# Performance work log

Hardware: AMD Instinct MI355X
Metric: run time of the kernel (lower is better)

## Reference

```python
import jax, jax.numpy as jnp
import numpy as np

B, S, K, H = 512, 128, 4, 128  # batch, seq_len, interest_num, hidden_size
ROUTING_TIMES = 3
EPS = 1e-9


def setup_inputs() -> dict:
    key = jax.random.key(0)
    k1, k2 = jax.random.split(key)
    item_eb = jax.random.normal(k1, (B, S, H), dtype=jnp.float32)
    mask = jnp.ones((B, S), dtype=jnp.float32)
    # learned bilinear map parameter (bilinear_type == 2)
    w = jax.random.normal(k2, (1, S, K * H, H), dtype=jnp.float32) * 0.02
    return {"item_eb": item_eb, "mask": mask, "w": w}


def _squash(cap):
    # cap: [B, K, 1, H]
    n = jnp.sum(cap * cap, axis=-1, keepdims=True)
    return (n / (1.0 + n) / jnp.sqrt(n + EPS)) * cap


def reference(item_eb, mask, w):
    # bilinear_type==2: sum(w[:, :S] * item_eb[:, :, None, :], axis=3)
    # expressed as an einsum to avoid the [B,S,K*H,H] intermediate
    item_eb_hat = jnp.einsum('bsh,sdh->bsd', item_eb, w[0])          # [B, S, K*H]
    item_eb_hat = item_eb_hat.reshape(B, S, K, H).transpose(0, 2, 1, 3)  # [B, K, S, H]
    hat_iter = jax.lax.stop_gradient(item_eb_hat)  # stop_grad=True

    atten_mask = jnp.broadcast_to(mask[:, None, :], (B, K, S))
    capsule_weight = jnp.zeros((B, K, S), dtype=item_eb.dtype)  # bilinear_type > 0

    interest_capsule = None
    for i in range(ROUTING_TIMES):
        # torch F.softmax with implicit dim on a 3D tensor -> dim=0 (legacy)
        sw = jax.nn.softmax(capsule_weight, axis=0)
        sw = jnp.where(atten_mask == 0, 0.0, sw)[:, :, None, :]  # [B, K, 1, S]
        src = hat_iter if i < 2 else item_eb_hat
        interest_capsule = _squash(jnp.matmul(sw, src))  # [B, K, 1, H]
        if i < 2:
            delta = jnp.matmul(hat_iter, interest_capsule.transpose(0, 1, 3, 2))  # [B,K,S,1]
            capsule_weight = capsule_weight + delta.reshape(B, K, S)

    return interest_capsule.reshape(B, K, H)
```

## Files before the change

kernel.cpp:

```cpp
#include <hip/hip_runtime.h>
#include <math.h>

#define BB 512
#define SS 128
#define KK 4
#define HH 128
#define DD 512

typedef __attribute__((ext_vector_type(8))) short bf16x8;
typedef __attribute__((ext_vector_type(4))) float f32x4;

__device__ __forceinline__ unsigned short f2bf(float f) {
  unsigned u = __float_as_uint(f);
  unsigned r = u + 0x7fffu + ((u >> 16) & 1u);
  return (unsigned short)(r >> 16);
}
__device__ __forceinline__ float bfhi(unsigned u) { return __uint_as_float(u & 0xffff0000u); }
__device__ __forceinline__ float bflo(unsigned u) { return __uint_as_float(u << 16); }
__device__ __forceinline__ unsigned pk2(float a, float b) {
  return (unsigned)f2bf(a) | ((unsigned)f2bf(b) << 16);
}

__global__ __launch_bounds__(256) void einsum_mfma(
    const float* __restrict__ A,
    const float* __restrict__ W,
    unsigned short* __restrict__ hat)
{
  __shared__ unsigned short Al[128 * 64];
  __shared__ unsigned short Wl[128 * 64];
  const int s  = blockIdx.x;
  const int b0 = (blockIdx.y & 3) * 128;
  const int dt = blockIdx.y >> 2;
  const int d0 = dt * 128;
  const int t  = threadIdx.x;
  const int lane = t & 63, wv = t >> 6;
  const int qm = wv & 1, qn = wv >> 1;
  const int n16 = lane & 15, kq = lane >> 4;
  const int r = t >> 1, cq = t & 1;

  f32x4 acc[4][4] = {};
  for (int ks = 0; ks < 128; ks += 64) {
    const float* ga = A + ((size_t)(b0 + r) * SS + s) * HH + ks + cq * 32;
    const float* gw = W + ((size_t)s * DD + d0 + r) * HH + ks + cq * 32;
    #pragma unroll
    for (int j = 0; j < 4; j++) {
      float4 a0 = *(const float4*)(ga + 8 * j);
      float4 a1 = *(const float4*)(ga + 8 * j + 4);
      float4 w0 = *(const float4*)(gw + 8 * j);
      float4 w1 = *(const float4*)(gw + 8 * j + 4);
      const int goff = ((cq * 4 + j + r) & 7) * 8;
      uint4 pa, pw;
      pa.x = pk2(a0.x, a0.y); pa.y = pk2(a0.z, a0.w);
      pa.z = pk2(a1.x, a1.y); pa.w = pk2(a1.z, a1.w);
      pw.x = pk2(w0.x, w0.y); pw.y = pk2(w0.z, w0.w);
      pw.z = pk2(w1.x, w1.y); pw.w = pk2(w1.z, w1.w);
      *(uint4*)&Al[r * 64 + goff] = pa;
      *(uint4*)&Wl[r * 64 + goff] = pw;
    }
    __syncthreads();
    #pragma unroll
    for (int kk = 0; kk < 2; kk++) {
      bf16x8 af[4], bfr[4];
      #pragma unroll
      for (int i = 0; i < 4; i++) {
        const int ra = qm * 64 + i * 16 + n16;
        const int rb = qn * 64 + i * 16 + n16;
        af[i]  = *(const bf16x8*)&Wl[ra * 64 + ((kk * 4 + kq + ra) & 7) * 8];
        bfr[i] = *(const bf16x8*)&Al[rb * 64 + ((kk * 4 + kq + rb) & 7) * 8];
      }
      #pragma unroll
      for (int i = 0; i < 4; i++)
        #pragma unroll
        for (int j = 0; j < 4; j++)
          acc[i][j] = __builtin_amdgcn_mfma_f32_16x16x32_bf16(af[i], bfr[j], acc[i][j], 0, 0, 0);
    }
    __syncthreads();
  }

  #pragma unroll
  for (int j = 0; j < 4; j++) {
    const int b = b0 + qn * 64 + j * 16 + n16;
    unsigned short* orow = hat + (((size_t)b * KK + dt) * SS + s) * HH;
    #pragma unroll
    for (int i = 0; i < 4; i++) {
      const int h = qm * 64 + i * 16 + kq * 4;
      ushort4 o;
      o.x = f2bf(acc[i][j][0]); o.y = f2bf(acc[i][j][1]);
      o.z = f2bf(acc[i][j][2]); o.w = f2bf(acc[i][j][3]);
      *(ushort4*)(orow + h) = o;
    }
  }
}

__global__ __launch_bounds__(256) void softmax_k(
    const float* __restrict__ cw, float* __restrict__ sw)
{
  __shared__ float T[512 * 33];
  __shared__ float red[2][8][32];
  const int s0 = blockIdx.x * 32, k = blockIdx.y, t = threadIdx.x;
  const int bg = t >> 3, c = t & 7;

  #pragma unroll
  for (int i = 0; i < 16; i++) {
    const int b = i * 32 + bg;
    float4 v = *(const float4*)(cw + ((size_t)b * KK + k) * SS + s0 + c * 4);
    float* Tr = &T[b * 33 + c * 4];
    Tr[0] = v.x; Tr[1] = v.y; Tr[2] = v.z; Tr[3] = v.w;
  }
  __syncthreads();

  const int sc = t & 31, grp = t >> 5;
  float mx = -3.4e38f;
  #pragma unroll 8
  for (int i = 0; i < 64; i++)
    mx = fmaxf(mx, T[(grp * 64 + i) * 33 + sc]);
  red[0][grp][sc] = mx;
  __syncthreads();
  float mall = red[0][0][sc];
  #pragma unroll
  for (int g = 1; g < 8; g++) mall = fmaxf(mall, red[0][g][sc]);
  float sm = 0.f;
  #pragma unroll 8
  for (int i = 0; i < 64; i++) {
    float* p = &T[(grp * 64 + i) * 33 + sc];
    float e = __expf(*p - mall);
    *p = e; sm += e;
  }
  red[1][grp][sc] = sm;
  __syncthreads();
  float tot = 0.f;
  #pragma unroll
  for (int g = 0; g < 8; g++) tot += red[1][g][sc];
  const float inv = 1.f / tot;
  #pragma unroll 8
  for (int i = 0; i < 64; i++)
    T[(grp * 64 + i) * 33 + sc] *= inv;
  __syncthreads();

  #pragma unroll
  for (int i = 0; i < 16; i++) {
    const int b = i * 32 + bg;
    const float* Tr = &T[b * 33 + c * 4];
    *(float4*)(sw + ((size_t)b * KK + k) * SS + s0 + c * 4) =
        make_float4(Tr[0], Tr[1], Tr[2], Tr[3]);
  }
}

__global__ __launch_bounds__(256) void routing_k(
    const unsigned short* __restrict__ hat, const float* __restrict__ mask,
    const float* __restrict__ sw_in, float* __restrict__ cw,
    float* __restrict__ out, int mode)
{
  __shared__ unsigned short hat_l[128 * 136];
  __shared__ float sw_l[128];
  __shared__ float4 red4[8][32];
  __shared__ float4 cq4[32];
  const int b = blockIdx.x, k = blockIdx.y, t = threadIdx.x;

  if (t < 128) {
    const float mk = mask[(size_t)b * SS + t];
    sw_l[t] = (mode == 0)
      ? ((mk == 0.f) ? 0.f : (1.f / 512.f))
      : ((mk == 0.f) ? 0.f : sw_in[((size_t)b * KK + k) * SS + t]);
  }
  const uint4* hp = (const uint4*)(hat + ((size_t)b * KK + k) * SS * HH);
  #pragma unroll
  for (int j = 0; j < 8; j++) {
    const int f = t + 256 * j;
    const int s = f >> 4, c = f & 15;
    *(uint4*)&hat_l[s * 136 + c * 8] = hp[f];
  }
  __syncthreads();

  {
    const int h4 = t & 31, sg = t >> 5;
    float4 a = make_float4(0.f, 0.f, 0.f, 0.f);
    #pragma unroll 4
    for (int i = 0; i < 16; i++) {
      const int s = sg * 16 + i;
      uint2 v = *(const uint2*)&hat_l[s * 136 + h4 * 4];
      float wv = sw_l[s];
      a.x = fmaf(wv, bflo(v.x), a.x);
      a.y = fmaf(wv, bfhi(v.x), a.y);
      a.z = fmaf(wv, bflo(v.y), a.z);
      a.w = fmaf(wv, bfhi(v.y), a.w);
    }
    red4[sg][h4] = a;
  }
  __syncthreads();

  if (t < 32) {
    float4 cap = red4[0][t];
    #pragma unroll
    for (int sg = 1; sg < 8; sg++) {
      float4 r = red4[sg][t];
      cap.x += r.x; cap.y += r.y; cap.z += r.z; cap.w += r.w;
    }
    float sq = cap.x * cap.x + cap.y * cap.y + cap.z * cap.z + cap.w * cap.w;
    #pragma unroll
    for (int o = 16; o; o >>= 1) sq += __shfl_xor(sq, o);
    const float n = sq;
    const float fac = n / (1.f + n) / sqrtf(n + 1e-9f);
    cap.x *= fac; cap.y *= fac; cap.z *= fac; cap.w *= fac;
    cq4[t] = cap;
    if (mode == 2)
      ((float4*)(out + ((size_t)b * KK + k) * HH))[t] = cap;
  }
  __syncthreads();

  if (mode < 2) {
    const int s = t >> 1, hh = t & 1;
    const uint4* row = (const uint4*)&hat_l[s * 136 + hh * 64];
    float d = 0.f;
    #pragma unroll
    for (int j = 0; j < 8; j++) {
      uint4 v = row[j];
      float4 qa = cq4[hh * 16 + 2 * j];
      float4 qb = cq4[hh * 16 + 2 * j + 1];
      d += bflo(v.x) * qa.x + bfhi(v.x) * qa.y
         + bflo(v.y) * qa.z + bfhi(v.y) * qa.w
         + bflo(v.z) * qb.x + bfhi(v.z) * qb.y
         + bflo(v.w) * qb.z + bfhi(v.w) * qb.w;
    }
    d += __shfl_xor(d, 1);
    if (hh == 0) {
      float* p = cw + ((size_t)b * KK + k) * SS + s;
      if (mode == 0) *p = d; else *p += d;
    }
  }
}

extern "C" void kernel_launch(void* const* d_in, const int* in_sizes, int n_in,
                              void* d_out, int out_size, void* d_ws, size_t ws_size,
                              hipStream_t stream) {
  const float* item_eb = (const float*)d_in[0];
  const float* mask    = (const float*)d_in[1];
  const float* w       = (const float*)d_in[2];
  float* out = (float*)d_out;

  char* ws = (char*)d_ws;
  unsigned short* hat_bf = (unsigned short*)ws;
  float* cw  = (float*)(ws + 67108864);
  float* swb = (float*)(ws + 68157440);

  einsum_mfma<<<dim3(128, 16), 256, 0, stream>>>(item_eb, w, hat_bf);

  routing_k<<<dim3(BB, KK), 256, 0, stream>>>(hat_bf, mask, nullptr, cw, out, 0);
  softmax_k<<<dim3(4, KK), 256, 0, stream>>>(cw, swb);
  routing_k<<<dim3(BB, KK), 256, 0, stream>>>(hat_bf, mask, swb, cw, out, 1);
  softmax_k<<<dim3(4, KK), 256, 0, stream>>>(cw, swb);
  routing_k<<<dim3(BB, KK), 256, 0, stream>>>(hat_bf, mask, swb, cw, out, 2);
}
```

Before: 196.2 us.

## Pre-convert inputs to bf16 and loop over interests per routing block

Adds a prep kernel that converts item_eb to bf16 in an s-major transposed layout and converts w to bf16. This lets the einsum kernel load contiguous bf16 tiles instead of doing strided fp32 loads with in-kernel packing. The routing kernel now handles all four interests of a batch row in one block, double-buffering the next interest's hat tile through registers into shared memory. The cost is an extra launch and an extra pass over roughly 50MB of input to write about 25MB, plus fewer and larger routing blocks that use more LDS.

```diff
diff --git a/kernel.cpp b/kernel.cpp
--- a/kernel.cpp
+++ b/kernel.cpp
@@ -17,13 +17,37 @@
 }
 __device__ __forceinline__ float bfhi(unsigned u) { return __uint_as_float(u & 0xffff0000u); }
 __device__ __forceinline__ float bflo(unsigned u) { return __uint_as_float(u << 16); }
-__device__ __forceinline__ unsigned pk2(float a, float b) {
-  return (unsigned)f2bf(a) | ((unsigned)f2bf(b) << 16);
+
+__global__ __launch_bounds__(256) void prep_k(
+    const float* __restrict__ item, const float* __restrict__ w,
+    unsigned short* __restrict__ item_t, unsigned short* __restrict__ w_bf)
+{
+  const int blk = blockIdx.x, t = threadIdx.x;
+  if (blk < 8192) {
+    const int rid = blk * 8 + (t >> 5);
+    const int b = rid >> 7, s = rid & 127;
+    const int c = t & 31;
+    float4 v = ((const float4*)(item + (size_t)rid * HH))[c];
+    ushort4 o;
+    o.x = f2bf(v.x); o.y = f2bf(v.y); o.z = f2bf(v.z); o.w = f2bf(v.w);
+    ((ushort4*)(item_t + ((size_t)s * BB + b) * HH))[c] = o;
+  } else {
+    size_t base = (size_t)(blk - 8192) * 2048 + t;
+    const float4* src = (const float4*)w;
+    ushort4* dst = (ushort4*)w_bf;
+    #pragma unroll
+    for (int j = 0; j < 8; j++) {
+      float4 v = src[base + 256 * j];
+      ushort4 o;
+      o.x = f2bf(v.x); o.y = f2bf(v.y); o.z = f2bf(v.z); o.w = f2bf(v.w);
+      dst[base + 256 * j] = o;
+    }
+  }
 }
 
 __global__ __launch_bounds__(256) void einsum_mfma(
-    const float* __restrict__ A,
-    const float* __restrict__ W,
+    const unsigned short* __restrict__ At,
+    const unsigned short* __restrict__ W,
     unsigned short* __restrict__ hat)
 {
   __shared__ unsigned short Al[128 * 64];
@@ -36,26 +60,21 @@
   const int lane = t & 63, wv = t >> 6;
   const int qm = wv & 1, qn = wv >> 1;
   const int n16 = lane & 15, kq = lane >> 4;
-  const int r = t >> 1, cq = t & 1;
+  const int sr = t >> 3, sc = t & 7;
+
+  const unsigned short* Abase = At + ((size_t)s * BB + b0) * HH;
+  const unsigned short* Wbase = W + ((size_t)s * DD + d0) * HH;
 
   f32x4 acc[4][4] = {};
   for (int ks = 0; ks < 128; ks += 64) {
-    const float* ga = A + ((size_t)(b0 + r) * SS + s) * HH + ks + cq * 32;
-    const float* gw = W + ((size_t)s * DD + d0 + r) * HH + ks + cq * 32;
     #pragma unroll
     for (int j = 0; j < 4; j++) {
-      float4 a0 = *(const float4*)(ga + 8 * j);
-      float4 a1 = *(const float4*)(ga + 8 * j + 4);
-      float4 w0 = *(const float4*)(gw + 8 * j);
-      float4 w1 = *(const float4*)(gw + 8 * j + 4);
-      const int goff = ((cq * 4 + j + r) & 7) * 8;
-      uint4 pa, pw;
-      pa.x = pk2(a0.x, a0.y); pa.y = pk2(a0.z, a0.w);
-      pa.z = pk2(a1.x, a1.y); pa.w = pk2(a1.z, a1.w);
-      pw.x = pk2(w0.x, w0.y); pw.y = pk2(w0.z, w0.w);
-      pw.z = pk2(w1.x, w1.y); pw.w = pk2(w1.z, w1.w);
-      *(uint4*)&Al[r * 64 + goff] = pa;
-      *(uint4*)&Wl[r * 64 + goff] = pw;
+      const int r = sr + 32 * j;
+      uint4 va = *(const uint4*)(Abase + (size_t)r * HH + ks + sc * 8);
+      uint4 vw = *(const uint4*)(Wbase + (size_t)r * HH + ks + sc * 8);
+      const int goff = ((sc + r) & 7) * 8;
+      *(uint4*)&Al[r * 64 + goff] = va;
+      *(uint4*)&Wl[r * 64 + goff] = vw;
     }
     __syncthreads();
     #pragma unroll
@@ -151,82 +170,116 @@
     const float* __restrict__ sw_in, float* __restrict__ cw,
     float* __restrict__ out, int mode)
 {
-  __shared__ unsigned short hat_l[128 * 136];
-  __shared__ float sw_l[128];
+  __shared__ unsigned short hat_l[2][128 * 136];
+  __shared__ float sw_l[4][128];
   __shared__ float4 red4[8][32];
   __shared__ float4 cq4[32];
-  const int b = blockIdx.x, k = blockIdx.y, t = threadIdx.x;
-
-  if (t < 128) {
-    const float mk = mask[(size_t)b * SS + t];
-    sw_l[t] = (mode == 0)
-      ? ((mk == 0.f) ? 0.f : (1.f / 512.f))
-      : ((mk == 0.f) ? 0.f : sw_in[((size_t)b * KK + k) * SS + t]);
-  }
-  const uint4* hp = (const uint4*)(hat + ((size_t)b * KK + k) * SS * HH);
-  #pragma unroll
-  for (int j = 0; j < 8; j++) {
-    const int f = t + 256 * j;
-    const int s = f >> 4, c = f & 15;
-    *(uint4*)&hat_l[s * 136 + c * 8] = hp[f];
-  }
-  __syncthreads();
+  const int b = blockIdx.x, t = threadIdx.x;
 
   {
-    const int h4 = t & 31, sg = t >> 5;
-    float4 a = make_float4(0.f, 0.f, 0.f, 0.f);
-    #pragma unroll 4
-    for (int i = 0; i < 16; i++) {
-      const int s = sg * 16 + i;
-      uint2 v = *(const uint2*)&hat_l[s * 136 + h4 * 4];
-      float wv = sw_l[s];
-      a.x = fmaf(wv, bflo(v.x), a.x);
-      a.y = fmaf(wv, bfhi(v.x), a.y);
-      a.z = fmaf(wv, bflo(v.y), a.z);
-      a.w = fmaf(wv, bfhi(v.y), a.w);
-    }
-    red4[sg][h4] = a;
-  }
-  __syncthreads();
-
-  if (t < 32) {
-    float4 cap = red4[0][t];
-    #pragma unroll
-    for (int sg = 1; sg < 8; sg++) {
-      float4 r = red4[sg][t];
-      cap.x += r.x; cap.y += r.y; cap.z += r.z; cap.w += r.w;
-    }
-    float sq = cap.x * cap.x + cap.y * cap.y + cap.z * cap.z + cap.w * cap.w;
-    #pragma unroll
-    for (int o = 16; o; o >>= 1) sq += __shfl_xor(sq, o);
-    const float n = sq;
-    const float fac = n / (1.f + n) / sqrtf(n + 1e-9f);
-    cap.x *= fac; cap.y *= fac; cap.z *= fac; cap.w *= fac;
-    cq4[t] = cap;
-    if (mode == 2)
-      ((float4*)(out + ((size_t)b * KK + k) * HH))[t] = cap;
-  }
-  __syncthreads();
-
-  if (mode < 2) {
-    const int s = t >> 1, hh = t & 1;
-    const uint4* row = (const uint4*)&hat_l[s * 136 + hh * 64];
-    float d = 0.f;
+    const float mk = mask[(size_t)b * SS + (t & 127)];
+    if (mode == 0) {
+      if (t < 128) {
+        const float v = (mk == 0.f) ? 0.f : (1.f / 512.f);
+        #pragma unroll
+        for (int k = 0; k < 4; k++) sw_l[k][t] = v;
+      }
+    } else {
+      const float* sp = sw_in + (size_t)b * 512;
+      float v0 = sp[t], v1 = sp[t + 256];
+      sw_l[t >> 7][t & 127]       = (mk == 0.f) ? 0.f : v0;
+      sw_l[2 + (t >> 7)][t & 127] = (mk == 0.f) ? 0.f : v1;
+    }
+  }
+
+  const uint4* hbase = (const uint4*)(hat + (size_t)b * KK * SS * HH);
+  const int src = t >> 4, scc = t & 15;
+
+  {
+    const uint4* hp = hbase;
     #pragma unroll
     for (int j = 0; j < 8; j++) {
-      uint4 v = row[j];
-      float4 qa = cq4[hh * 16 + 2 * j];
-      float4 qb = cq4[hh * 16 + 2 * j + 1];
-      d += bflo(v.x) * qa.x + bfhi(v.x) * qa.y
-         + bflo(v.y) * qa.z + bfhi(v.y) * qa.w
-         + bflo(v.z) * qb.x + bfhi(v.z) * qb.y
-         + bflo(v.w) * qb.z + bfhi(v.w) * qb.w;
-    }
-    d += __shfl_xor(d, 1);
-    if (hh == 0) {
-      float* p = cw + ((size_t)b * KK + k) * SS + s;
-      if (mode == 0) *p = d; else *p += d;
-    }
+      const int f = t + 256 * j;
+      *(uint4*)&hat_l[0][(f >> 4) * 136 + (f & 15) * 8] = hp[f];
+    }
+  }
+  __syncthreads();
+
+  for (int k = 0; k < 4; k++) {
+    const int cur = k & 1;
+    uint4 stg[8];
+    if (k < 3) {
+      const uint4* hp = hbase + (size_t)(k + 1) * 2048;
+      #pragma unroll
+      for (int j = 0; j < 8; j++) stg[j] = hp[t + 256 * j];
+    }
+
+    {
+      const int h4 = t & 31, sg = t >> 5;
+      float4 a = make_float4(0.f, 0.f, 0.f, 0.f);
+      #pragma unroll 4
+      for (int i = 0; i < 16; i++) {
+        const int s = sg * 16 + i;
+        uint2 v = *(const uint2*)&hat_l[cur][s * 136 + h4 * 4];
+        float wv = sw_l[k][s];
+        a.x = fmaf(wv, bflo(v.x), a.x);
+        a.y = fmaf(wv, bfhi(v.x), a.y);
+        a.z = fmaf(wv, bflo(v.y), a.z);
+        a.w = fmaf(wv, bfhi(v.y), a.w);
+      }
+      red4[sg][h4] = a;
+    }
+    __syncthreads();
+
+    if (t < 32) {
+      float4 cap = red4[0][t];
+      #pragma unroll
+      for (int sg = 1; sg < 8; sg++) {
+        float4 r = red4[sg][t];
+        cap.x += r.x; cap.y += r.y; cap.z += r.z; cap.w += r.w;
+      }
+      float sq = cap.x * cap.x + cap.y * cap.y + cap.z * cap.z + cap.w * cap.w;
+      #pragma unroll
+      for (int o = 16; o; o >>= 1) sq += __shfl_xor(sq, o);
+      const float n = sq;
+      const float fac = n / (1.f + n) / sqrtf(n + 1e-9f);
+      cap.x *= fac; cap.y *= fac; cap.z *= fac; cap.w *= fac;
+      cq4[t] = cap;
+      if (mode == 2)
+        ((float4*)(out + ((size_t)b * KK + k) * HH))[t] = cap;
+    }
+    __syncthreads();
+
+    if (mode < 2) {
+      const int s = t >> 1, hh = t & 1;
+      const uint4* row = (const uint4*)&hat_l[cur][s * 136 + hh * 64];
+      float d = 0.f;
+      #pragma unroll
+      for (int j = 0; j < 8; j++) {
+        uint4 v = row[j];
+        float4 qa = cq4[hh * 16 + 2 * j];
+        float4 qb = cq4[hh * 16 + 2 * j + 1];
+        d += bflo(v.x) * qa.x + bfhi(v.x) * qa.y
+           + bflo(v.y) * qa.z + bfhi(v.y) * qa.w
+           + bflo(v.z) * qb.x + bfhi(v.z) * qb.y
+           + bflo(v.w) * qb.z + bfhi(v.w) * qb.w;
+      }
+      d += __shfl_xor(d, 1);
+      if (hh == 0) {
+        float* p = cw + ((size_t)b * KK + k) * SS + s;
+        if (mode == 0) *p = d; else *p += d;
+      }
+    }
+
+    if (k < 3) {
+      const int nxt = cur ^ 1;
+      #pragma unroll
+      for (int j = 0; j < 8; j++) {
+        const int f = t + 256 * j;
+        *(uint4*)&hat_l[nxt][(f >> 4) * 136 + (f & 15) * 8] = stg[j];
+      }
+    }
+    __syncthreads();
   }
 }
 
@@ -239,15 +292,18 @@
   float* out = (float*)d_out;
 
   char* ws = (char*)d_ws;
-  unsigned short* hat_bf = (unsigned short*)ws;
-  float* cw  = (float*)(ws + 67108864);
-  float* swb = (float*)(ws + 68157440);
-
-  einsum_mfma<<<dim3(128, 16), 256, 0, stream>>>(item_eb, w, hat_bf);
-
-  routing_k<<<dim3(BB, KK), 256, 0, stream>>>(hat_bf, mask, nullptr, cw, out, 0);
+  unsigned short* hat_bf  = (unsigned short*)ws;
+  unsigned short* item_t  = (unsigned short*)(ws + 67108864);
+  unsigned short* w_bf    = (unsigned short*)(ws + 83886080);
+  float* cw  = (float*)(ws + 100663296);
+  float* swb = (float*)(ws + 101711872);
+
+  prep_k<<<dim3(9216), 256, 0, stream>>>(item_eb, w, item_t, w_bf);
+  einsum_mfma<<<dim3(128, 16), 256, 0, stream>>>(item_t, w_bf, hat_bf);
+
+  routing_k<<<dim3(BB), 256, 0, stream>>>(hat_bf, mask, nullptr, cw, out, 0);
   softmax_k<<<dim3(4, KK), 256, 0, stream>>>(cw, swb);
-  routing_k<<<dim3(BB, KK), 256, 0, stream>>>(hat_bf, mask, swb, cw, out, 1);
+  routing_k<<<dim3(BB), 256, 0, stream>>>(hat_bf, mask, swb, cw, out, 1);
   softmax_k<<<dim3(4, KK), 256, 0, stream>>>(cw, swb);
-  routing_k<<<dim3(BB, KK), 256, 0, stream>>>(hat_bf, mask, swb, cw, out, 2);
-}
+  routing_k<<<dim3(BB), 256, 0, stream>>>(hat_bf, mask, swb, cw, out, 2);
+}
```

After: 230.6 us. 1.18x slower.
